# Performance work log

Hardware: AMD Instinct MI355X
Metric: run time of the kernel (lower is better)

Reference implementation:

```python
import jax, jax.numpy as jnp
import numpy as np

S = 128          # shared sequence length of v/q/a/k
D = 512          # model dim
H = 8            # n_heads
W = D // H       # head width (becomes the v/q/a einsum axes)
NUM = S // 8     # num_v = num_q = num_a = num_k
SCALE = float(np.sqrt(H))  # source divides by sqrt(a.size(-1)) == sqrt(n_heads)


def _heads(x):
    # split_last(x,(H,-1)).transpose(1,2) on a 2D (S,D) tensor -> (S, W, H)
    return x.reshape(S, H, W).transpose(0, 2, 1)


def setup_inputs() -> dict:
    key = jax.random.key(0)
    ks = jax.random.split(key, 24)
    d = {}
    for i, n in enumerate(['v', 'q', 'a', 'k']):
        d[n] = jax.random.normal(ks[i], (S, D), jnp.float32)
    for n in ['v_mask', 'q_mask', 'a_mask', 'k_mask']:
        d[n] = jnp.ones((S,), jnp.bool_)
    wnames = ['Wv', 'Wq', 'Wa', 'Wk', 'Wvo', 'Wqo', 'Wao', 'Wko']
    bnames = ['bv', 'bq', 'ba', 'bk', 'bvo', 'bqo', 'bao', 'bko']
    for i, (wn, bn) in enumerate(zip(wnames, bnames)):
        d[wn] = jax.random.normal(ks[4 + 2 * i], (D, D), jnp.float32) / np.sqrt(D)
        d[bn] = jax.random.normal(ks[5 + 2 * i], (D,), jnp.float32) * 0.01
    return d


def reference(v, q, a, k, v_mask, q_mask, a_mask, k_mask,
              Wv, bv, Wq, bq, Wa, ba, Wk, bk,
              Wvo, bvo, Wqo, bqo, Wao, bao, Wko, bko):
    # input projections (torch Linear: x @ W.T + b)
    vp = v @ Wv.T + bv
    qp = q @ Wq.T + bq
    ap = a @ Wa.T + ba
    kp = k @ Wk.T + bk
    # output projections are applied to the already-projected tensors
    vo = vp @ Wvo.T + bvo
    qo = qp @ Wqo.T + bqo
    ao = ap @ Wao.T + bao
    ko = kp @ Wko.T + bko
    tv, tq, ta, tk = map(_heads, (vp, qp, ap, kp))      # (S, W, H)
    tvo, tqo, tao, tko = map(_heads, (vo, qo, ao, ko))  # (S, W, H)
    # trilinear scores: in source labels b=1, h=S, v/q/a in W, w=H
    att = jnp.einsum('sic,sjc,slc->sijl', tv, tq, ta) / SCALE   # (S, W, W, W)
    att1 = jnp.einsum('sic,sjc,slc->sijl', tv, tq, tk) / SCALE  # (S, W, W, W)
    # joint softmax over the flat num_v*num_q*num_a axis (flat memory reshape,
    # exactly like torch .view); dropout p=0.0 -> identity
    scores = jax.nn.softmax(att.reshape(-1, H, NUM * NUM * NUM), axis=-1)
    scores = scores.reshape(-1, H, NUM, NUM, NUM)  # stored as self.scores in torch
    # output contractions use the UNNORMALIZED att1 (as in the source)
    v_res = jnp.einsum('sijl,sic->isc', att1, tvo).reshape(1, W, S * H)
    q_res = jnp.einsum('sijl,sjc->jsc', att1, tqo).reshape(1, W, S * H)
    a_res = jnp.einsum('sijl,slc->lsc', att1, tao).reshape(1, W, S * H)
    k_res = tko[None].reshape(1, S, W * H)
    return (v_res, q_res, a_res, k_res, scores)
```

## Files before the change

kernel.cpp:

```cpp
#include <hip/hip_runtime.h>

#define INV_SCALE 0.35355339059327373f
#define LOG2E 1.4426950408889634f

struct Proj4Args {
  const float* x[4];
  const float* w[4];
  const float* b[4];
  float* y[4];
};

__global__ __launch_bounds__(256) void proj4_kernel(Proj4Args A) {
  __shared__ float SH[6176];
  const int blk = blockIdx.x;
  const int p = blk >> 7;
  const int dbase = ((blk >> 1) & 63) * 8;
  const int shalf = (blk & 1) * 64;
  const int t = threadIdx.x;
  const int s = t & 63;
  const int g = t >> 6;
  float* WL = SH;
  float(*XT)[65] = (float(*)[65])(SH + 4096);
  {
    const float4* wg = (const float4*)(A.w[p] + dbase * 512);
    float4* wl4 = (float4*)WL;
#pragma unroll
    for (int r = 0; r < 4; ++r) wl4[t + r * 256] = wg[t + r * 256];
  }
  const float* xg = A.x[p] + shalf * 512;
  const int row = t >> 3;
  const int col = t & 7;
  float acc[2] = {0.f, 0.f};
  float4 pre[2];
#pragma unroll
  for (int r = 0; r < 2; ++r)
    pre[r] = ((const float4*)(xg + (row + r * 32) * 512))[col];
  for (int c = 0; c < 16; ++c) {
    __syncthreads();
#pragma unroll
    for (int r = 0; r < 2; ++r) {
      float4 f = pre[r];
      int rr = row + r * 32;
      XT[col * 4 + 0][rr] = f.x;
      XT[col * 4 + 1][rr] = f.y;
      XT[col * 4 + 2][rr] = f.z;
      XT[col * 4 + 3][rr] = f.w;
    }
    __syncthreads();
    if (c + 1 < 16) {
#pragma unroll
      for (int r = 0; r < 2; ++r)
        pre[r] = ((const float4*)(xg + (row + r * 32) * 512))[(c + 1) * 8 + col];
    }
#pragma unroll
    for (int k4 = 0; k4 < 8; ++k4) {
      float xv0 = XT[k4 * 4 + 0][s];
      float xv1 = XT[k4 * 4 + 1][s];
      float xv2 = XT[k4 * 4 + 2][s];
      float xv3 = XT[k4 * 4 + 3][s];
#pragma unroll
      for (int di = 0; di < 2; ++di) {
        const float4 wv =
            *(const float4*)&WL[(g * 2 + di) * 512 + c * 32 + k4 * 4];
        acc[di] = fmaf(wv.x, xv0, acc[di]);
        acc[di] = fmaf(wv.y, xv1, acc[di]);
        acc[di] = fmaf(wv.z, xv2, acc[di]);
        acc[di] = fmaf(wv.w, xv3, acc[di]);
      }
    }
  }
  const float* bp = A.b[p] + dbase + g * 2;
  *(float2*)(A.y[p] + (shalf + s) * 512 + dbase + g * 2) =
      make_float2(acc[0] + bp[0], acc[1] + bp[1]);
}

template <int CHUNK>
__device__ __forceinline__ void gemm8_body(const float* xg, const float* wg_p,
                                           const float* bp, int dbase, int t,
                                           float* SH, float o[4]) {
  const int s = t & 127;
  const int h = t >> 7;
  float* WL = SH;
  float(*XT)[129] = (float(*)[129])(SH + 4096);
  {
    const float4* wg = (const float4*)(wg_p + dbase * 512);
    float4* wl4 = (float4*)WL;
#pragma unroll
    for (int r = 0; r < 4; ++r) wl4[t + r * 256] = wg[t + r * 256];
  }
  constexpr int C4 = CHUNK / 4;
  constexpr int RPT = C4 / 2;
  constexpr int NCH = 512 / CHUNK;
  constexpr int RSTEP = 256 / C4;
  const int row = t / C4;
  const int col = t % C4;
  float acc[4] = {0.f, 0.f, 0.f, 0.f};
  float4 pre[RPT];
#pragma unroll
  for (int r = 0; r < RPT; ++r)
    pre[r] = ((const float4*)(xg + (row + r * RSTEP) * 512))[col];
  for (int c = 0; c < NCH; ++c) {
    __syncthreads();
#pragma unroll
    for (int r = 0; r < RPT; ++r) {
      float4 f = pre[r];
      int rr = row + r * RSTEP;
      XT[col * 4 + 0][rr] = f.x;
      XT[col * 4 + 1][rr] = f.y;
      XT[col * 4 + 2][rr] = f.z;
      XT[col * 4 + 3][rr] = f.w;
    }
    __syncthreads();
    if (c + 1 < NCH) {
#pragma unroll
      for (int r = 0; r < RPT; ++r)
        pre[r] =
            ((const float4*)(xg + (row + r * RSTEP) * 512))[(c + 1) * C4 + col];
    }
#pragma unroll
    for (int k4 = 0; k4 < C4; ++k4) {
      float xv0 = XT[k4 * 4 + 0][s];
      float xv1 = XT[k4 * 4 + 1][s];
      float xv2 = XT[k4 * 4 + 2][s];
      float xv3 = XT[k4 * 4 + 3][s];
#pragma unroll
      for (int di = 0; di < 4; ++di) {
        const float4 wv =
            *(const float4*)&WL[(h * 4 + di) * 512 + c * CHUNK + k4 * 4];
        acc[di] = fmaf(wv.x, xv0, acc[di]);
        acc[di] = fmaf(wv.y, xv1, acc[di]);
        acc[di] = fmaf(wv.z, xv2, acc[di]);
        acc[di] = fmaf(wv.w, xv3, acc[di]);
      }
    }
  }
#pragma unroll
  for (int di = 0; di < 4; ++di) o[di] = acc[di] + bp[dbase + h * 4 + di];
}

struct FusedArgs {
  const float* w2[4];
  const float* b2[4];
  const float* vp;
  const float* qp;
  const float* ap;
  const float* kp;
  float* out;
};

__device__ __forceinline__ void proj2_direct_body(const FusedArgs& F, int blk,
                                                  int t, float* SH) {
  const int p = blk >> 6;
  const int dbase = (blk & 63) * 8;
  const float* xsrc[4] = {F.vp, F.qp, F.ap, F.kp};
  float o[4];
  gemm8_body<16>(xsrc[p], F.w2[p], F.b2[p], dbase, t, SH, o);
  const int s = t & 127;
  const int h = t >> 7;
  const int c_head = dbase >> 6;
  const int i0 = (dbase & 63) + h * 4;
  if (p == 3) {
#pragma unroll
    for (int di = 0; di < 4; ++di)
      F.out[196608 + s * 512 + (i0 + di) * 8 + c_head] = o[di];
    return;
  }
  const float* fac = (p == 0) ? F.vp : (p == 1) ? F.qp : F.kp;
  const float* S0 = (p == 0) ? F.qp : F.vp;
  const float* S1 = (p == 2) ? F.qp : F.kp;
  __syncthreads();
  float* Sm = SH;
#pragma unroll
  for (int m = 0; m < 2; ++m) {
    const float* M = m ? S1 : S0;
#pragma unroll
    for (int cc = 0; cc < 4; ++cc) {
      const int c = h * 4 + cc;
      const float4* r4 = (const float4*)(M + s * 512 + c * 64);
      float sum = 0.f;
#pragma unroll
      for (int u = 0; u < 16; ++u) {
        float4 f = r4[u];
        sum += (f.x + f.y) + (f.z + f.w);
      }
      Sm[m * 1024 + s * 8 + c] = sum;
    }
  }
  __syncthreads();
  float prod[8];
#pragma unroll
  for (int c = 0; c < 8; ++c)
    prod[c] = Sm[s * 8 + c] * Sm[1024 + s * 8 + c];
#pragma unroll
  for (int di = 0; di < 4; ++di) {
    const int i = i0 + di;
    float A1 = 0.f;
#pragma unroll
    for (int c = 0; c < 8; ++c)
      A1 = fmaf(fac[s * 512 + c * 64 + i], prod[c], A1);
    F.out[p * 65536 + i * 1024 + s * 8 + c_head] = o[di] * (A1 * INV_SCALE);
  }
}

__device__ __forceinline__ void scores_body(const float* __restrict__ vp,
                                            const float* __restrict__ qp,
                                            const float* __restrict__ ap,
                                            float* __restrict__ out, int b,
                                            int t, float* SH) {
  const int s = b >> 4;
  const int i0 = (b & 15) * 4;
  float* tqL = SH;
  float* taL = SH + 512;
  float* uL = SH + 1024;
  float(*redS)[4] = (float(*)[4])(SH + 1056);
  if (t < 128)
    ((float4*)tqL)[t] = ((const float4*)(qp + s * 512))[t];
  else
    ((float4*)taL)[t - 128] = ((const float4*)(ap + s * 512))[t - 128];
  if (t < 32) {
    int ii = t >> 3, c = t & 7;
    uL[t] = vp[s * 512 + c * 64 + i0 + ii] * (INV_SCALE * LOG2E);
  }
  __syncthreads();
  const int wid = t >> 6, ln = t & 63;
  const int jb = 16 * wid + (ln >> 4);
  const int lq = (ln & 15) * 4;
  float acc[4][16];
#pragma unroll
  for (int ii = 0; ii < 4; ++ii)
#pragma unroll
    for (int x = 0; x < 16; ++x) acc[ii][x] = 0.f;
#pragma unroll
  for (int c = 0; c < 8; ++c) {
    const float* tq_c = &tqL[c * 64 + jb];
    float tj0 = tq_c[0];
    float tj1 = tq_c[4];
    float tj2 = tq_c[8];
    float tj3 = tq_c[12];
    float4 ta4 = *reinterpret_cast<const float4*>(&taL[c * 64 + lq]);
#pragma unroll
    for (int ii = 0; ii < 4; ++ii) {
      float uv = uL[ii * 8 + c];
      float m0 = uv * tj0;
      float m1 = uv * tj1;
      float m2 = uv * tj2;
      float m3 = uv * tj3;
      acc[ii][0] = fmaf(m0, ta4.x, acc[ii][0]);
      acc[ii][1] = fmaf(m0, ta4.y, acc[ii][1]);
      acc[ii][2] = fmaf(m0, ta4.z, acc[ii][2]);
      acc[ii][3] = fmaf(m0, ta4.w, acc[ii][3]);
      acc[ii][4] = fmaf(m1, ta4.x, acc[ii][4]);
      acc[ii][5] = fmaf(m1, ta4.y, acc[ii][5]);
      acc[ii][6] = fmaf(m1, ta4.z, acc[ii][6]);
      acc[ii][7] = fmaf(m1, ta4.w, acc[ii][7]);
      acc[ii][8] = fmaf(m2, ta4.x, acc[ii][8]);
      acc[ii][9] = fmaf(m2, ta4.y, acc[ii][9]);
      acc[ii][10] = fmaf(m2, ta4.z, acc[ii][10]);
      acc[ii][11] = fmaf(m2, ta4.w, acc[ii][11]);
      acc[ii][12] = fmaf(m3, ta4.x, acc[ii][12]);
      acc[ii][13] = fmaf(m3, ta4.y, acc[ii][13]);
      acc[ii][14] = fmaf(m3, ta4.z, acc[ii][14]);
      acc[ii][15] = fmaf(m3, ta4.w, acc[ii][15]);
    }
  }
#pragma unroll
  for (int ii = 0; ii < 4; ++ii) {
    float sl = 0.f;
#pragma unroll
    for (int x = 0; x < 16; ++x) {
      float e = exp2f(acc[ii][x]);
      acc[ii][x] = e;
      sl += e;
    }
#pragma unroll
    for (int o = 32; o; o >>= 1) sl += __shfl_xor(sl, o);
    if (ln == 0) redS[ii][wid] = sl;
  }
  __syncthreads();
  const long sbase = 262144L + (long)s * 262144 + (long)i0 * 4096;
#pragma unroll
  for (int ii = 0; ii < 4; ++ii) {
    float tot = (redS[ii][0] + redS[ii][1]) + (redS[ii][2] + redS[ii][3]);
    float sc = 1.0f / tot;
    float* ob = out + sbase + ii * 4096 + wid * 1024 + ln * 4;
#pragma unroll
    for (int k = 0; k < 4; ++k) {
      *reinterpret_cast<float4*>(ob + k * 256) =
          make_float4(acc[ii][k * 4 + 0] * sc, acc[ii][k * 4 + 1] * sc,
                      acc[ii][k * 4 + 2] * sc, acc[ii][k * 4 + 3] * sc);
    }
  }
}

__global__ __launch_bounds__(256) void fused_kernel(FusedArgs F) {
  __shared__ float SH[6160];
  const int b = blockIdx.x;
  if (b < 256)
    proj2_direct_body(F, b, threadIdx.x, SH);
  else
    scores_body(F.vp, F.qp, F.ap, F.out, b - 256, threadIdx.x, SH);
}

extern "C" void kernel_launch(void* const* d_in, const int* in_sizes, int n_in,
                              void* d_out, int out_size, void* d_ws, size_t ws_size,
                              hipStream_t stream) {
  int wb = 8;
  if (n_in >= 5 && in_sizes[4] == 262144) wb = 4;
  const float* W[8];
  const float* B[8];
  for (int i = 0; i < 8; ++i) {
    W[i] = (const float*)d_in[wb + 2 * i];
    B[i] = (const float*)d_in[wb + 2 * i + 1];
  }
  float* ws = (float*)d_ws;
  float* vp = ws;
  float* qp = ws + 65536;
  float* ap = ws + 131072;
  float* kp = ws + 196608;
  float* out = (float*)d_out;

  Proj4Args a1;
  for (int i = 0; i < 4; ++i) {
    a1.x[i] = (const float*)d_in[i];
    a1.w[i] = W[i];
    a1.b[i] = B[i];
  }
  a1.y[0] = vp; a1.y[1] = qp; a1.y[2] = ap; a1.y[3] = kp;
  hipLaunchKernelGGL(proj4_kernel, dim3(512), dim3(256), 0, stream, a1);

  FusedArgs F;
  for (int i = 0; i < 4; ++i) {
    F.w2[i] = W[4 + i];
    F.b2[i] = B[4 + i];
  }
  F.vp = vp; F.qp = qp; F.ap = ap; F.kp = kp; F.out = out;
  hipLaunchKernelGGL(fused_kernel, dim3(2304), dim3(256), 0, stream, F);
}
```

Before: 225.6 us.

## Assign one softmax row per wavefront to drop cross-wave reduction and barrier

```diff
diff --git a/kernel.cpp b/kernel.cpp
--- a/kernel.cpp
+++ b/kernel.cpp
@@ -211,84 +211,53 @@
   const int i0 = (b & 15) * 4;
   float* tqL = SH;
   float* taL = SH + 512;
-  float* uL = SH + 1024;
-  float(*redS)[4] = (float(*)[4])(SH + 1056);
   if (t < 128)
     ((float4*)tqL)[t] = ((const float4*)(qp + s * 512))[t];
   else
     ((float4*)taL)[t - 128] = ((const float4*)(ap + s * 512))[t - 128];
-  if (t < 32) {
-    int ii = t >> 3, c = t & 7;
-    uL[t] = vp[s * 512 + c * 64 + i0 + ii] * (INV_SCALE * LOG2E);
-  }
+  const int wid = t >> 6, ln = t & 63;
+  const int i = i0 + wid;
+  const float* vrow = vp + s * 512 + i;
+  float u[8];
+#pragma unroll
+  for (int c = 0; c < 8; ++c) u[c] = vrow[c * 64] * (INV_SCALE * LOG2E);
   __syncthreads();
-  const int wid = t >> 6, ln = t & 63;
-  const int jb = 16 * wid + (ln >> 4);
+  const int jb = ln >> 4;
   const int lq = (ln & 15) * 4;
-  float acc[4][16];
-#pragma unroll
-  for (int ii = 0; ii < 4; ++ii)
-#pragma unroll
-    for (int x = 0; x < 16; ++x) acc[ii][x] = 0.f;
+  float4 acc[16];
+#pragma unroll
+  for (int k = 0; k < 16; ++k) acc[k] = make_float4(0.f, 0.f, 0.f, 0.f);
 #pragma unroll
   for (int c = 0; c < 8; ++c) {
+    const float4 ta4 = *reinterpret_cast<const float4*>(&taL[c * 64 + lq]);
     const float* tq_c = &tqL[c * 64 + jb];
-    float tj0 = tq_c[0];
-    float tj1 = tq_c[4];
-    float tj2 = tq_c[8];
-    float tj3 = tq_c[12];
-    float4 ta4 = *reinterpret_cast<const float4*>(&taL[c * 64 + lq]);
-#pragma unroll
-    for (int ii = 0; ii < 4; ++ii) {
-      float uv = uL[ii * 8 + c];
-      float m0 = uv * tj0;
-      float m1 = uv * tj1;
-      float m2 = uv * tj2;
-      float m3 = uv * tj3;
-      acc[ii][0] = fmaf(m0, ta4.x, acc[ii][0]);
-      acc[ii][1] = fmaf(m0, ta4.y, acc[ii][1]);
-      acc[ii][2] = fmaf(m0, ta4.z, acc[ii][2]);
-      acc[ii][3] = fmaf(m0, ta4.w, acc[ii][3]);
-      acc[ii][4] = fmaf(m1, ta4.x, acc[ii][4]);
-      acc[ii][5] = fmaf(m1, ta4.y, acc[ii][5]);
-      acc[ii][6] = fmaf(m1, ta4.z, acc[ii][6]);
-      acc[ii][7] = fmaf(m1, ta4.w, acc[ii][7]);
-      acc[ii][8] = fmaf(m2, ta4.x, acc[ii][8]);
-      acc[ii][9] = fmaf(m2, ta4.y, acc[ii][9]);
-      acc[ii][10] = fmaf(m2, ta4.z, acc[ii][10]);
-      acc[ii][11] = fmaf(m2, ta4.w, acc[ii][11]);
-      acc[ii][12] = fmaf(m3, ta4.x, acc[ii][12]);
-      acc[ii][13] = fmaf(m3, ta4.y, acc[ii][13]);
-      acc[ii][14] = fmaf(m3, ta4.z, acc[ii][14]);
-      acc[ii][15] = fmaf(m3, ta4.w, acc[ii][15]);
-    }
-  }
-#pragma unroll
-  for (int ii = 0; ii < 4; ++ii) {
-    float sl = 0.f;
-#pragma unroll
-    for (int x = 0; x < 16; ++x) {
-      float e = exp2f(acc[ii][x]);
-      acc[ii][x] = e;
-      sl += e;
-    }
-#pragma unroll
-    for (int o = 32; o; o >>= 1) sl += __shfl_xor(sl, o);
-    if (ln == 0) redS[ii][wid] = sl;
-  }
-  __syncthreads();
-  const long sbase = 262144L + (long)s * 262144 + (long)i0 * 4096;
-#pragma unroll
-  for (int ii = 0; ii < 4; ++ii) {
-    float tot = (redS[ii][0] + redS[ii][1]) + (redS[ii][2] + redS[ii][3]);
-    float sc = 1.0f / tot;
-    float* ob = out + sbase + ii * 4096 + wid * 1024 + ln * 4;
-#pragma unroll
-    for (int k = 0; k < 4; ++k) {
-      *reinterpret_cast<float4*>(ob + k * 256) =
-          make_float4(acc[ii][k * 4 + 0] * sc, acc[ii][k * 4 + 1] * sc,
-                      acc[ii][k * 4 + 2] * sc, acc[ii][k * 4 + 3] * sc);
-    }
+    const float uc = u[c];
+#pragma unroll
+    for (int k = 0; k < 16; ++k) {
+      float m = uc * tq_c[4 * k];
+      acc[k].x = fmaf(m, ta4.x, acc[k].x);
+      acc[k].y = fmaf(m, ta4.y, acc[k].y);
+      acc[k].z = fmaf(m, ta4.z, acc[k].z);
+      acc[k].w = fmaf(m, ta4.w, acc[k].w);
+    }
+  }
+  float sl = 0.f;
+#pragma unroll
+  for (int k = 0; k < 16; ++k) {
+    acc[k].x = exp2f(acc[k].x);
+    acc[k].y = exp2f(acc[k].y);
+    acc[k].z = exp2f(acc[k].z);
+    acc[k].w = exp2f(acc[k].w);
+    sl += (acc[k].x + acc[k].y) + (acc[k].z + acc[k].w);
+  }
+#pragma unroll
+  for (int o = 32; o; o >>= 1) sl += __shfl_xor(sl, o);
+  const float sc = 1.0f / sl;
+  float* ob = out + 262144L + (long)s * 262144 + (long)i * 4096 + ln * 4;
+#pragma unroll
+  for (int k = 0; k < 16; ++k) {
+    *reinterpret_cast<float4*>(ob + k * 256) =
+        make_float4(acc[k].x * sc, acc[k].y * sc, acc[k].z * sc, acc[k].w * sc);
   }
 }
 
```

Result: no change. 224.8 us (-0.3%).
